# Kernel tuning notes

Hardware: AMD Instinct MI355X
Metric: run time of the kernel (lower is better)

The kernel has to match this reference:

```python
import jax, jax.numpy as jnp
import numpy as np

DIM = 128
HEADS = 4
G = 16           # group_size (window)
POS_DIM = (DIM // 4) // 4  # 8, DPB hidden dim
EPS = 1e-5


def _ln(x, g, b):
    m = x.mean(-1, keepdims=True)
    v = ((x - m) ** 2).mean(-1, keepdims=True)
    return (x - m) * jax.lax.rsqrt(v + EPS) * g + b


def _rel_index(Gh, Gw):
    # relative_position_index as in the torch code (static, numpy)
    coords = np.stack(np.meshgrid(np.arange(Gh), np.arange(Gw), indexing='ij'))  # [2,Gh,Gw]
    cf = coords.reshape(2, -1)
    rel = (cf[:, :, None] - cf[:, None, :]).transpose(1, 2, 0)  # [N,N,2]
    rel[..., 0] += Gh - 1
    rel[..., 1] += Gw - 1
    rel[..., 0] *= 2 * Gw - 1
    return rel.sum(-1)  # [N,N]


def _bias_coords(Gh, Gw):
    bh = np.arange(1 - Gh, Gh)
    bw = np.arange(1 - Gw, Gw)
    b = np.stack(np.meshgrid(bh, bw, indexing='ij')).reshape(2, -1).T  # [(2Gh-1)(2Gw-1),2]
    return b.astype(np.float32)


def setup_inputs() -> dict:
    key = jax.random.key(0)
    ks = jax.random.split(key, 16)
    C, P, h = DIM, POS_DIM, HEADS
    s = 0.02
    return {
        'x': jax.random.normal(ks[0], (2, 256 * 256, C), jnp.float32),
        'norm1_g': jnp.ones((C,), jnp.float32),
        'norm1_b': jnp.zeros((C,), jnp.float32),
        'qkv_w': jax.random.normal(ks[1], (3 * C, C), jnp.float32) * s,
        'qkv_b': jnp.zeros((3 * C,), jnp.float32),
        'pp_w': jax.random.normal(ks[2], (P, 2), jnp.float32) * s,
        'pp_b': jnp.zeros((P,), jnp.float32),
        'l1_g': jnp.ones((P,), jnp.float32), 'l1_b': jnp.zeros((P,), jnp.float32),
        'f1_w': jax.random.normal(ks[3], (P, P), jnp.float32) * s,
        'f1_b': jnp.zeros((P,), jnp.float32),
        'l2_g': jnp.ones((P,), jnp.float32), 'l2_b': jnp.zeros((P,), jnp.float32),
        'f2_w': jax.random.normal(ks[4], (P, P), jnp.float32) * s,
        'f2_b': jnp.zeros((P,), jnp.float32),
        'l3_g': jnp.ones((P,), jnp.float32), 'l3_b': jnp.zeros((P,), jnp.float32),
        'f3_w': jax.random.normal(ks[5], (h, P), jnp.float32) * s,
        'f3_b': jnp.zeros((h,), jnp.float32),
        'H': 256,
        'W': 256,
    }


def reference(x, norm1_g, norm1_b, qkv_w, qkv_b, pp_w, pp_b,
              l1_g, l1_b, f1_w, f1_b, l2_g, l2_b, f2_w, f2_b,
              l3_g, l3_b, f3_w, f3_b, H, W):
    B, L, C = x.shape
    h = HEADS
    d = C // h
    N = G * G
    shortcut = x
    xn = _ln(x, norm1_g, norm1_b).reshape(B, H, W, C)
    # SDA window partition: (B, H/G, G, W/G, G, C) -> (B*nW, G*G, C)
    xw = xn.reshape(B, H // G, G, W // G, G, C).transpose(0, 1, 3, 2, 4, 5).reshape(-1, N, C)
    qkv = (xw @ qkv_w.T + qkv_b).reshape(-1, N, 3, h, d).transpose(2, 0, 3, 1, 4)
    q, k, v = qkv[0] * (d ** -0.5), qkv[1], qkv[2]
    attn = jnp.einsum('bhnd,bhmd->bhnm', q, k)  # [B_, h, N, N]
    # DynamicPosBias (residual=False): pos3(pos2(pos1(pos_proj(biases))))
    biases = jnp.asarray(_bias_coords(G, G))  # [(2G-1)^2, 2]
    pos = biases @ pp_w.T + pp_b
    pos = jax.nn.relu(_ln(pos, l1_g, l1_b)) @ f1_w.T + f1_b
    pos = jax.nn.relu(_ln(pos, l2_g, l2_b)) @ f2_w.T + f2_b
    pos = jax.nn.relu(_ln(pos, l3_g, l3_b)) @ f3_w.T + f3_b  # [(2G-1)^2, h]
    rpi = jnp.asarray(_rel_index(G, G).reshape(-1))
    bias = pos[rpi].reshape(N, N, h).transpose(2, 0, 1)  # [h, N, N]
    attn = jax.nn.softmax(attn + bias[None], axis=-1)
    out = jnp.einsum('bhnm,bhmd->bhnd', attn, v).transpose(0, 2, 1, 3).reshape(-1, N, C)
    # reverse partition
    out = out.reshape(B, H // G, W // G, G, G, C).transpose(0, 1, 3, 2, 4, 5).reshape(B, L, C)
    return shortcut + out
```

## Files before the change

### kernel.cpp

```cpp
#include <hip/hip_runtime.h>
#include <hip/hip_bf16.h>

typedef __bf16 bf16_t;
typedef __bf16 bf16x2 __attribute__((ext_vector_type(2)));
typedef __bf16 bf16x4 __attribute__((ext_vector_type(4)));
typedef __bf16 bf16x8 __attribute__((ext_vector_type(8)));
typedef short s16x4 __attribute__((ext_vector_type(4)));
typedef float f32x2 __attribute__((ext_vector_type(2)));
typedef float f32x4 __attribute__((ext_vector_type(4)));
typedef unsigned int u32;

#define MFMA16(a, b, c) __builtin_amdgcn_mfma_f32_16x16x32_bf16(a, b, c, 0, 0, 0)

static __device__ inline f32x4 mfma_pv(bf16x4 a, bf16x4 b, f32x4 c) {
#if __has_builtin(__builtin_amdgcn_mfma_f32_16x16x16_bf16)
    return __builtin_amdgcn_mfma_f32_16x16x16_bf16(a, b, c, 0, 0, 0);
#elif __has_builtin(__builtin_amdgcn_mfma_f32_16x16x16bf16_1k)
    return __builtin_amdgcn_mfma_f32_16x16x16bf16_1k(
        __builtin_bit_cast(s16x4, a), __builtin_bit_cast(s16x4, b), c, 0, 0, 0);
#else
    f32x4 d;
    asm volatile("v_mfma_f32_16x16x16_bf16 %0, %1, %2, %3"
                 : "=v"(d) : "v"(a), "v"(b), "v"(c));
    return d;
#endif
}

__device__ inline float ldf(const void* p, int i, int f32) {
    return f32 ? ((const float*)p)[i] : (float)((const bf16_t*)p)[i];
}

__device__ inline void ln8(float* p, const void* g, const void* b, int f32) {
    float m = 0.f;
#pragma unroll
    for (int i = 0; i < 8; ++i) m += p[i];
    m *= 0.125f;
    float v = 0.f;
#pragma unroll
    for (int i = 0; i < 8; ++i) { float d = p[i] - m; v += d * d; }
    v *= 0.125f;
    float r = rsqrtf(v + 1e-5f);
#pragma unroll
    for (int i = 0; i < 8; ++i)
        p[i] = fmaxf((p[i] - m) * r * ldf(g, i, f32) + ldf(b, i, f32), 0.f);
}

__global__ __launch_bounds__(256) void prep_all(
    const void* __restrict__ xv, bf16_t* __restrict__ xn,
    int* __restrict__ flags,
    const void* __restrict__ qw, const void* __restrict__ qb,
    const void* __restrict__ ng, const void* __restrict__ nb,
    bf16_t* __restrict__ Wp, float* __restrict__ uu, float* __restrict__ tt,
    const void* __restrict__ ppw, const void* __restrict__ ppb,
    const void* __restrict__ l1g, const void* __restrict__ l1b,
    const void* __restrict__ f1w, const void* __restrict__ f1b,
    const void* __restrict__ l2g, const void* __restrict__ l2b,
    const void* __restrict__ f2w, const void* __restrict__ f2b,
    const void* __restrict__ l3g, const void* __restrict__ l3b,
    const void* __restrict__ f3w, const void* __restrict__ f3b,
    float* __restrict__ pos) {
    const int tid = threadIdx.x;
    const int lane = tid & 63;
    u32 pv = ((const u32*)xv)[lane];
    int pf = (((pv >> 7) & 0xFFu) >= 0x90u) || (((pv >> 23) & 0xFFu) >= 0x90u);
    const int f32 = __any(pf) ? 1 : 0;
    const int bid = blockIdx.x;
    if (bid == 0 && tid == 0) flags[0] = f32;

    if (bid >= 100) {
        const int sub = lane & 15;
        const int t = (bid - 100) * 16 + (tid >> 6) * 4 + (lane >> 4);
        float f[8];
        if (f32) {
            const float* p = (const float*)xv + t * 128 + sub * 8;
            f32x4 a = *(const f32x4*)p;
            f32x4 b = *(const f32x4*)(p + 4);
#pragma unroll
            for (int e = 0; e < 4; ++e) { f[e] = a[e]; f[4 + e] = b[e]; }
        } else {
            bf16x8 v = *(const bf16x8*)((const bf16_t*)xv + t * 128 + sub * 8);
#pragma unroll
            for (int e = 0; e < 8; ++e) f[e] = (float)v[e];
        }
        float s = 0.f, s2 = 0.f;
#pragma unroll
        for (int e = 0; e < 8; ++e) { s += f[e]; s2 += f[e] * f[e]; }
#pragma unroll
        for (int off = 8; off >= 1; off >>= 1) {
            s += __shfl_xor(s, off, 64);
            s2 += __shfl_xor(s2, off, 64);
        }
        float mu = s * (1.f / 128.f);
        float r = rsqrtf(s2 * (1.f / 128.f) - mu * mu + 1e-5f);
        bf16x8 h;
#pragma unroll
        for (int e = 0; e < 8; ++e) h[e] = (bf16_t)((f[e] - mu) * r);
        *(bf16x8*)(xn + t * 128 + sub * 8) = h;
        return;
    }

    if (bid < 96) {
        int j = bid * 4 + (tid >> 6);
        int l = lane;
        float g0 = ldf(ng, l, f32),  g1 = ldf(ng, l + 64, f32);
        float b0 = ldf(nb, l, f32),  b1 = ldf(nb, l + 64, f32);
        float w0 = ldf(qw, j * 128 + l, f32), w1 = ldf(qw, j * 128 + l + 64, f32);
        float wg0 = w0 * g0, wg1 = w1 * g1;
        Wp[j * 128 + l] = (bf16_t)wg0;
        Wp[j * 128 + l + 64] = (bf16_t)wg1;
        float su = wg0 + wg1;
        float st = w0 * b0 + w1 * b1;
#pragma unroll
        for (int off = 32; off >= 1; off >>= 1) {
            su += __shfl_xor(su, off, 64);
            st += __shfl_xor(st, off, 64);
        }
        if (l == 0) { uu[j] = su; tt[j] = st + ldf(qb, j, f32); }
        return;
    }

    int r = (bid - 96) * 256 + tid;
    if (r >= 961) return;
    float bh = (float)(r / 31) - 15.f;
    float bw = (float)(r % 31) - 15.f;
    float p[8], q[8];
#pragma unroll
    for (int i = 0; i < 8; ++i)
        p[i] = ldf(ppw, i * 2, f32) * bh + ldf(ppw, i * 2 + 1, f32) * bw + ldf(ppb, i, f32);
    ln8(p, l1g, l1b, f32);
#pragma unroll
    for (int o = 0; o < 8; ++o) {
        float s = ldf(f1b, o, f32);
#pragma unroll
        for (int i = 0; i < 8; ++i) s += p[i] * ldf(f1w, o * 8 + i, f32);
        q[o] = s;
    }
    ln8(q, l2g, l2b, f32);
#pragma unroll
    for (int o = 0; o < 8; ++o) {
        float s = ldf(f2b, o, f32);
#pragma unroll
        for (int i = 0; i < 8; ++i) s += q[i] * ldf(f2w, o * 8 + i, f32);
        p[o] = s;
    }
    ln8(p, l3g, l3b, f32);
#pragma unroll
    for (int o = 0; o < 4; ++o) {
        float s = ldf(f3b, o, f32);
#pragma unroll
        for (int i = 0; i < 8; ++i) s += p[i] * ldf(f3w, o * 8 + i, f32);
        pos[r * 4 + o] = s;
    }
}

template <int XN>
__global__ __launch_bounds__(256, 4) void win_attn(
    const void* __restrict__ xv, const bf16_t* __restrict__ xnp,
    const bf16_t* __restrict__ Wp, const float* __restrict__ uu,
    const float* __restrict__ tt, const float* __restrict__ posg,
    const int* __restrict__ flags, void* __restrict__ outv) {
    __shared__ __align__(16) bf16_t k_s[256 * 40];
    __shared__ __align__(16) bf16_t vT_s[32 * 264];
    __shared__ bf16_t pos_s[962];
    __shared__ float tt_s[96];
    __shared__ float uu_s[XN ? 2 : 96];
    __shared__ float mu_s[XN ? 2 : 256];
    __shared__ float r_s[XN ? 2 : 256];

    const int f32 = flags[0];
    const int tid = threadIdx.x;
    const int lane = tid & 63;
    const int w = tid >> 6;
    const int l15 = lane & 15;
    const int quad = lane >> 4;
    const int bid = blockIdx.x;
    const int head = (bid >> 3) & 3;
    const int wi = (bid & 7) | ((bid >> 5) << 3);
    const int bi = wi >> 8;
    const int wh = (wi >> 4) & 15, ww = wi & 15;
    const int xbase = bi * (256 * 256 * 128);

    if (tid < 96) {
        int sg = tid >> 5, dd = tid & 31;
        tt_s[tid] = tt[sg * 128 + head * 32 + dd];
        if (!XN) uu_s[tid] = uu[sg * 128 + head * 32 + dd];
    }
    for (int r = tid; r < 961; r += 256) pos_s[r] = (bf16_t)posg[r * 4 + head];

    if (!XN) {
#pragma unroll
        for (int it = 0; it < 4; ++it) {
            int i = w * 64 + it * 16 + (lane >> 2);
            int gi = xbase + ((wh * 16 + (i >> 4)) * 256 + ww * 16 + (i & 15)) * 128;
            float s = 0.f, s2 = 0.f;
            if (f32) {
                const f32x4* p4 = (const f32x4*)((const float*)xv + gi);
#pragma unroll
                for (int c = 0; c < 4; ++c) {
                    f32x4 a = p4[(c * 4 + (lane & 3)) * 2];
                    f32x4 b = p4[(c * 4 + (lane & 3)) * 2 + 1];
#pragma unroll
                    for (int e = 0; e < 4; ++e) { s += a[e] + b[e]; s2 += a[e] * a[e] + b[e] * b[e]; }
                }
            } else {
                const bf16_t* p = (const bf16_t*)xv + gi;
#pragma unroll
                for (int c = 0; c < 4; ++c) {
                    bf16x8 v = *(const bf16x8*)(p + (c * 4 + (lane & 3)) * 8);
#pragma unroll
                    for (int e = 0; e < 8; ++e) { float f = (float)v[e]; s += f; s2 += f * f; }
                }
            }
            s  += __shfl_xor(s, 1, 4);  s  += __shfl_xor(s, 2, 4);
            s2 += __shfl_xor(s2, 1, 4); s2 += __shfl_xor(s2, 2, 4);
            if ((lane & 3) == 0) {
                float mu = s * (1.f / 128.f);
                mu_s[i] = mu;
                r_s[i] = rsqrtf(s2 * (1.f / 128.f) - mu * mu + 1e-5f);
            }
        }
    }
    __syncthreads();

    int axi[4];
#pragma unroll
    for (int mt = 0; mt < 4; ++mt) {
        int i = w * 64 + mt * 16 + l15;
        axi[mt] = xbase + ((wh * 16 + (i >> 4)) * 256 + ww * 16 + (i & 15)) * 128;
    }
    const float qscale = 0.17677669529663689f;
    bf16x8 qB[4];

#pragma unroll 1
    for (int sel = 0; sel < 3; ++sel) {
        f32x4 acc[2][4];
#pragma unroll
        for (int nt = 0; nt < 2; ++nt)
#pragma unroll
            for (int mt = 0; mt < 4; ++mt) acc[nt][mt] = f32x4{0.f, 0.f, 0.f, 0.f};
        const bf16_t* bw0 = Wp + (sel * 128 + head * 32 + l15) * 128;
        const bf16_t* bw1 = bw0 + 16 * 128;
#pragma unroll
        for (int ks = 0; ks < 4; ++ks) {
            int ko = ks * 32 + quad * 8;
            bf16x8 af[4];
            if (XN) {
#pragma unroll
                for (int mt = 0; mt < 4; ++mt)
                    af[mt] = *(const bf16x8*)(xnp + axi[mt] + ko);
            } else if (f32) {
#pragma unroll
                for (int mt = 0; mt < 4; ++mt) {
                    const float* pp = (const float*)xv + axi[mt] + ko;
                    f32x4 u0 = *(const f32x4*)pp;
                    f32x4 u1 = *(const f32x4*)(pp + 4);
                    bf16x8 t;
#pragma unroll
                    for (int e = 0; e < 4; ++e) { t[e] = (bf16_t)u0[e]; t[e + 4] = (bf16_t)u1[e]; }
                    af[mt] = t;
                }
            } else {
#pragma unroll
                for (int mt = 0; mt < 4; ++mt)
                    af[mt] = *(const bf16x8*)((const bf16_t*)xv + axi[mt] + ko);
            }
            bf16x8 b0 = *(const bf16x8*)(bw0 + ko);
            bf16x8 b1 = *(const bf16x8*)(bw1 + ko);
#pragma unroll
            for (int mt = 0; mt < 4; ++mt) {
                acc[0][mt] = MFMA16(af[mt], b0, acc[0][mt]);
                acc[1][mt] = MFMA16(af[mt], b1, acc[1][mt]);
            }
        }
#pragma unroll
        for (int nt = 0; nt < 2; ++nt) {
            int d = nt * 16 + l15;
            float tj = tt_s[sel * 32 + d];
            float uj = XN ? 0.f : uu_s[sel * 32 + d];
#pragma unroll
            for (int mt = 0; mt < 4; ++mt) {
                int tok0 = w * 64 + mt * 16 + quad * 4;
                float vv[4];
#pragma unroll
                for (int rg = 0; rg < 4; ++rg) {
                    int token = tok0 + rg;
                    if (XN) vv[rg] = acc[nt][mt][rg] + tj;
                    else    vv[rg] = r_s[token] * (acc[nt][mt][rg] - mu_s[token] * uj) + tj;
                }
                if (sel == 0) {
#pragma unroll
                    for (int rg = 0; rg < 4; ++rg)
                        k_s[(tok0 + rg) * 40 + d] = (bf16_t)(vv[rg] * qscale);
                } else if (sel == 1) {
#pragma unroll
                    for (int rg = 0; rg < 4; ++rg)
                        k_s[(tok0 + rg) * 40 + d] = (bf16_t)vv[rg];
                } else {
                    bf16x4 h = { (bf16_t)vv[0], (bf16_t)vv[1],
                                 (bf16_t)vv[2], (bf16_t)vv[3] };
                    *(bf16x4*)(vT_s + d * 264 + tok0) = h;
                }
            }
        }
        if (sel == 0) {
#pragma unroll
            for (int qt = 0; qt < 4; ++qt)
                qB[qt] = *(const bf16x8*)(k_s + (w * 64 + qt * 16 + l15) * 40 + quad * 8);
            __syncthreads();
        }
    }
    __syncthreads();

    f32x4 Oa[2][4];
#pragma unroll
    for (int np = 0; np < 2; ++np)
#pragma unroll
        for (int qt = 0; qt < 4; ++qt) Oa[np][qt] = f32x4{0.f, 0.f, 0.f, 0.f};
    float lsum[4] = {0.f, 0.f, 0.f, 0.f};

    const f32x4 zero4 = {0.f, 0.f, 0.f, 0.f};
    const int vinner = l15 + 15 - quad * 4;

    for (int kb = 0; kb < 8; ++kb) {
        bf16x4 pF[2][4];
#pragma unroll
        for (int nt = 0; nt < 2; ++nt) {
            bf16x8 kf = *(const bf16x8*)(k_s + (kb * 32 + nt * 16 + l15) * 40 + quad * 8);
            f32x4 S[4];
            __builtin_amdgcn_s_setprio(1);
#pragma unroll
            for (int qt = 0; qt < 4; ++qt) S[qt] = MFMA16(kf, qB[qt], zero4);
            __builtin_amdgcn_s_setprio(0);
#pragma unroll
            for (int qt = 0; qt < 4; ++qt) {
                int souter = (w * 4 + qt - kb * 2 - nt + 15) * 31;
                float p[4];
#pragma unroll
                for (int rg = 0; rg < 4; ++rg) {
                    float b = (float)pos_s[souter + vinner - rg];
                    p[rg] = __expf(S[qt][rg] + b);
                }
                lsum[qt] += (p[0] + p[1]) + (p[2] + p[3]);
                bf16x4 h = { (bf16_t)p[0], (bf16_t)p[1], (bf16_t)p[2], (bf16_t)p[3] };
                pF[nt][qt] = h;
            }
        }
#pragma unroll
        for (int np = 0; np < 2; ++np) {
            const bf16_t* vrow = vT_s + (np * 16 + l15) * 264 + kb * 32 + quad * 4;
            bf16x4 vf0 = *(const bf16x4*)vrow;
            bf16x4 vf1 = *(const bf16x4*)(vrow + 16);
            __builtin_amdgcn_s_setprio(1);
#pragma unroll
            for (int qt = 0; qt < 4; ++qt) {
                Oa[np][qt] = mfma_pv(vf0, pF[0][qt], Oa[np][qt]);
                Oa[np][qt] = mfma_pv(vf1, pF[1][qt], Oa[np][qt]);
            }
            __builtin_amdgcn_s_setprio(0);
        }
    }

    float inv[4];
#pragma unroll
    for (int qt = 0; qt < 4; ++qt) {
        float l = lsum[qt];
        l += __shfl_xor(l, 16, 64);
        l += __shfl_xor(l, 32, 64);
        inv[qt] = 1.f / l;
    }
#pragma unroll
    for (int np = 0; np < 2; ++np)
#pragma unroll
        for (int qt = 0; qt < 4; ++qt) {
            int go = xbase + ((wh * 16 + w * 4 + qt) * 256 + ww * 16 + l15) * 128 +
                     head * 32 + np * 16 + quad * 4;
            if (f32) {
                f32x4 res = *(const f32x4*)((const float*)xv + go);
                f32x4 o;
#pragma unroll
                for (int rg = 0; rg < 4; ++rg) o[rg] = Oa[np][qt][rg] * inv[qt] + res[rg];
                *(f32x4*)((float*)outv + go) = o;
            } else {
                bf16x4 res = *(const bf16x4*)((const bf16_t*)xv + go);
                bf16x4 o;
#pragma unroll
                for (int rg = 0; rg < 4; ++rg)
                    o[rg] = (bf16_t)(Oa[np][qt][rg] * inv[qt] + (float)res[rg]);
                *(bf16x4*)((bf16_t*)outv + go) = o;
            }
        }
}

extern "C" void kernel_launch(void* const* d_in, const int* in_sizes, int n_in,
                              void* d_out, int out_size, void* d_ws, size_t ws_size,
                              hipStream_t stream) {
    const void* x   = d_in[0];
    const void* ng  = d_in[1];
    const void* nb  = d_in[2];
    const void* qw  = d_in[3];
    const void* qb  = d_in[4];
    const void* ppw = d_in[5];
    const void* ppb = d_in[6];
    const void* l1g = d_in[7];
    const void* l1b = d_in[8];
    const void* f1w = d_in[9];
    const void* f1b = d_in[10];
    const void* l2g = d_in[11];
    const void* l2b = d_in[12];
    const void* f2w = d_in[13];
    const void* f2b = d_in[14];
    const void* l3g = d_in[15];
    const void* l3b = d_in[16];
    const void* f3w = d_in[17];
    const void* f3b = d_in[18];

    char* ws = (char*)d_ws;
    int*    flags = (int*)ws;
    bf16_t* Wp    = (bf16_t*)(ws + 16);
    float*  uu    = (float*)(ws + 98320);
    float*  tt    = (float*)(ws + 99856);
    float*  pos   = (float*)(ws + 101392);
    bf16_t* xn    = (bf16_t*)(ws + 116768);
    const int use_xn = (ws_size >= 116768 + 33554432u) ? 1 : 0;

    int prep_grid = use_xn ? 8292 : 100;
    prep_all<<<dim3(prep_grid), dim3(256), 0, stream>>>(
        x, xn, flags, qw, qb, ng, nb, Wp, uu, tt,
        ppw, ppb, l1g, l1b, f1w, f1b, l2g, l2b, f2w, f2b, l3g, l3b,
        f3w, f3b, pos);
    if (use_xn)
        win_attn<1><<<dim3(2048), dim3(256), 0, stream>>>(x, xn, Wp, uu, tt, pos,
                                                          flags, d_out);
    else
        win_attn<0><<<dim3(2048), dim3(256), 0, stream>>>(x, xn, Wp, uu, tt, pos,
                                                          flags, d_out);
}
```

Before: 270.8 us.

## Drop separate LayerNorm pass and fuse row stats into window attention kernel

After: 304.6 us. 1.12x slower.

```diff
diff --git a/kernel.cpp b/kernel.cpp
--- a/kernel.cpp
+++ b/kernel.cpp
@@ -46,8 +46,7 @@
 }
 
 __global__ __launch_bounds__(256) void prep_all(
-    const void* __restrict__ xv, bf16_t* __restrict__ xn,
-    int* __restrict__ flags,
+    const void* __restrict__ xv,
     const void* __restrict__ qw, const void* __restrict__ qb,
     const void* __restrict__ ng, const void* __restrict__ nb,
     bf16_t* __restrict__ Wp, float* __restrict__ uu, float* __restrict__ tt,
@@ -65,39 +64,6 @@
     int pf = (((pv >> 7) & 0xFFu) >= 0x90u) || (((pv >> 23) & 0xFFu) >= 0x90u);
     const int f32 = __any(pf) ? 1 : 0;
     const int bid = blockIdx.x;
-    if (bid == 0 && tid == 0) flags[0] = f32;
-
-    if (bid >= 100) {
-        const int sub = lane & 15;
-        const int t = (bid - 100) * 16 + (tid >> 6) * 4 + (lane >> 4);
-        float f[8];
-        if (f32) {
-            const float* p = (const float*)xv + t * 128 + sub * 8;
-            f32x4 a = *(const f32x4*)p;
-            f32x4 b = *(const f32x4*)(p + 4);
-#pragma unroll
-            for (int e = 0; e < 4; ++e) { f[e] = a[e]; f[4 + e] = b[e]; }
-        } else {
-            bf16x8 v = *(const bf16x8*)((const bf16_t*)xv + t * 128 + sub * 8);
-#pragma unroll
-            for (int e = 0; e < 8; ++e) f[e] = (float)v[e];
-        }
-        float s = 0.f, s2 = 0.f;
-#pragma unroll
-        for (int e = 0; e < 8; ++e) { s += f[e]; s2 += f[e] * f[e]; }
-#pragma unroll
-        for (int off = 8; off >= 1; off >>= 1) {
-            s += __shfl_xor(s, off, 64);
-            s2 += __shfl_xor(s2, off, 64);
-        }
-        float mu = s * (1.f / 128.f);
-        float r = rsqrtf(s2 * (1.f / 128.f) - mu * mu + 1e-5f);
-        bf16x8 h;
-#pragma unroll
-        for (int e = 0; e < 8; ++e) h[e] = (bf16_t)((f[e] - mu) * r);
-        *(bf16x8*)(xn + t * 128 + sub * 8) = h;
-        return;
-    }
 
     if (bid < 96) {
         int j = bid * 4 + (tid >> 6);
@@ -153,26 +119,22 @@
     }
 }
 
-template <int XN>
 __global__ __launch_bounds__(256, 4) void win_attn(
-    const void* __restrict__ xv, const bf16_t* __restrict__ xnp,
-    const bf16_t* __restrict__ Wp, const float* __restrict__ uu,
-    const float* __restrict__ tt, const float* __restrict__ posg,
-    const int* __restrict__ flags, void* __restrict__ outv) {
+    const void* __restrict__ xv, const bf16_t* __restrict__ Wp,
+    const float* __restrict__ uu, const float* __restrict__ tt,
+    const float* __restrict__ posg, void* __restrict__ outv) {
     __shared__ __align__(16) bf16_t k_s[256 * 40];
     __shared__ __align__(16) bf16_t vT_s[32 * 264];
     __shared__ bf16_t pos_s[962];
-    __shared__ float tt_s[96];
-    __shared__ float uu_s[XN ? 2 : 96];
-    __shared__ float mu_s[XN ? 2 : 256];
-    __shared__ float r_s[XN ? 2 : 256];
-
-    const int f32 = flags[0];
+
     const int tid = threadIdx.x;
     const int lane = tid & 63;
     const int w = tid >> 6;
     const int l15 = lane & 15;
     const int quad = lane >> 4;
+    u32 pvw = ((const u32*)xv)[lane];
+    int pfb = (((pvw >> 7) & 0xFFu) >= 0x90u) || (((pvw >> 23) & 0xFFu) >= 0x90u);
+    const int f32 = __any(pfb) ? 1 : 0;
     const int bid = blockIdx.x;
     const int head = (bid >> 3) & 3;
     const int wi = (bid & 7) | ((bid >> 5) << 3);
@@ -180,47 +142,40 @@
     const int wh = (wi >> 4) & 15, ww = wi & 15;
     const int xbase = bi * (256 * 256 * 128);
 
-    if (tid < 96) {
-        int sg = tid >> 5, dd = tid & 31;
-        tt_s[tid] = tt[sg * 128 + head * 32 + dd];
-        if (!XN) uu_s[tid] = uu[sg * 128 + head * 32 + dd];
-    }
     for (int r = tid; r < 961; r += 256) pos_s[r] = (bf16_t)posg[r * 4 + head];
 
-    if (!XN) {
-#pragma unroll
-        for (int it = 0; it < 4; ++it) {
-            int i = w * 64 + it * 16 + (lane >> 2);
-            int gi = xbase + ((wh * 16 + (i >> 4)) * 256 + ww * 16 + (i & 15)) * 128;
-            float s = 0.f, s2 = 0.f;
-            if (f32) {
-                const f32x4* p4 = (const f32x4*)((const float*)xv + gi);
-#pragma unroll
-                for (int c = 0; c < 4; ++c) {
-                    f32x4 a = p4[(c * 4 + (lane & 3)) * 2];
-                    f32x4 b = p4[(c * 4 + (lane & 3)) * 2 + 1];
-#pragma unroll
-                    for (int e = 0; e < 4; ++e) { s += a[e] + b[e]; s2 += a[e] * a[e] + b[e] * b[e]; }
-                }
-            } else {
-                const bf16_t* p = (const bf16_t*)xv + gi;
-#pragma unroll
-                for (int c = 0; c < 4; ++c) {
-                    bf16x8 v = *(const bf16x8*)(p + (c * 4 + (lane & 3)) * 8);
-#pragma unroll
-                    for (int e = 0; e < 8; ++e) { float f = (float)v[e]; s += f; s2 += f * f; }
-                }
-            }
-            s  += __shfl_xor(s, 1, 4);  s  += __shfl_xor(s, 2, 4);
-            s2 += __shfl_xor(s2, 1, 4); s2 += __shfl_xor(s2, 2, 4);
-            if ((lane & 3) == 0) {
-                float mu = s * (1.f / 128.f);
-                mu_s[i] = mu;
-                r_s[i] = rsqrtf(s2 * (1.f / 128.f) - mu * mu + 1e-5f);
-            }
-        }
-    }
-    __syncthreads();
+#pragma unroll
+    for (int it = 0; it < 4; ++it) {
+        int i = w * 64 + it * 16 + (lane >> 2);
+        int gi = xbase + ((wh * 16 + (i >> 4)) * 256 + ww * 16 + (i & 15)) * 128;
+        float s = 0.f, s2 = 0.f;
+        if (f32) {
+            const f32x4* p4 = (const f32x4*)((const float*)xv + gi);
+#pragma unroll
+            for (int c = 0; c < 4; ++c) {
+                f32x4 a = p4[(c * 4 + (lane & 3)) * 2];
+                f32x4 b = p4[(c * 4 + (lane & 3)) * 2 + 1];
+#pragma unroll
+                for (int e = 0; e < 4; ++e) { s += a[e] + b[e]; s2 += a[e] * a[e] + b[e] * b[e]; }
+            }
+        } else {
+            const bf16_t* p = (const bf16_t*)xv + gi;
+#pragma unroll
+            for (int c = 0; c < 4; ++c) {
+                bf16x8 v = *(const bf16x8*)(p + (c * 4 + (lane & 3)) * 8);
+#pragma unroll
+                for (int e = 0; e < 8; ++e) { float f = (float)v[e]; s += f; s2 += f * f; }
+            }
+        }
+        s  += __shfl_xor(s, 1, 4);  s  += __shfl_xor(s, 2, 4);
+        s2 += __shfl_xor(s2, 1, 4); s2 += __shfl_xor(s2, 2, 4);
+        if ((lane & 3) == 0) {
+            float mu = s * (1.f / 128.f);
+            float r = rsqrtf(s2 * (1.f / 128.f) - mu * mu + 1e-5f);
+            f32x2 st = { mu, r };
+            *(f32x2*)(k_s + i * 40 + 32) = st;
+        }
+    }
 
     int axi[4];
 #pragma unroll
@@ -233,6 +188,12 @@
 
 #pragma unroll 1
     for (int sel = 0; sel < 3; ++sel) {
+        float tjv[2], ujv[2];
+#pragma unroll
+        for (int nt = 0; nt < 2; ++nt) {
+            tjv[nt] = tt[sel * 128 + head * 32 + nt * 16 + l15];
+            ujv[nt] = uu[sel * 128 + head * 32 + nt * 16 + l15];
+        }
         f32x4 acc[2][4];
 #pragma unroll
         for (int nt = 0; nt < 2; ++nt)
@@ -244,11 +205,7 @@
         for (int ks = 0; ks < 4; ++ks) {
             int ko = ks * 32 + quad * 8;
             bf16x8 af[4];
-            if (XN) {
-#pragma unroll
-                for (int mt = 0; mt < 4; ++mt)
-                    af[mt] = *(const bf16x8*)(xnp + axi[mt] + ko);
-            } else if (f32) {
+            if (f32) {
 #pragma unroll
                 for (int mt = 0; mt < 4; ++mt) {
                     const float* pp = (const float*)xv + axi[mt] + ko;
@@ -273,20 +230,21 @@
             }
         }
 #pragma unroll
-        for (int nt = 0; nt < 2; ++nt) {
-            int d = nt * 16 + l15;
-            float tj = tt_s[sel * 32 + d];
-            float uj = XN ? 0.f : uu_s[sel * 32 + d];
-#pragma unroll
-            for (int mt = 0; mt < 4; ++mt) {
-                int tok0 = w * 64 + mt * 16 + quad * 4;
+        for (int mt = 0; mt < 4; ++mt) {
+            int tok0 = w * 64 + mt * 16 + quad * 4;
+            float mu4[4], r4[4];
+#pragma unroll
+            for (int rg = 0; rg < 4; ++rg) {
+                f32x2 st = *(const f32x2*)(k_s + (tok0 + rg) * 40 + 32);
+                mu4[rg] = st[0]; r4[rg] = st[1];
+            }
+#pragma unroll
+            for (int nt = 0; nt < 2; ++nt) {
+                int d = nt * 16 + l15;
                 float vv[4];
 #pragma unroll
-                for (int rg = 0; rg < 4; ++rg) {
-                    int token = tok0 + rg;
-                    if (XN) vv[rg] = acc[nt][mt][rg] + tj;
-                    else    vv[rg] = r_s[token] * (acc[nt][mt][rg] - mu_s[token] * uj) + tj;
-                }
+                for (int rg = 0; rg < 4; ++rg)
+                    vv[rg] = r4[rg] * (acc[nt][mt][rg] - mu4[rg] * ujv[nt]) + tjv[nt];
                 if (sel == 0) {
 #pragma unroll
                     for (int rg = 0; rg < 4; ++rg)
@@ -306,7 +264,6 @@
 #pragma unroll
             for (int qt = 0; qt < 4; ++qt)
                 qB[qt] = *(const bf16x8*)(k_s + (w * 64 + qt * 16 + l15) * 40 + quad * 8);
-            __syncthreads();
         }
     }
     __syncthreads();
@@ -415,23 +372,14 @@
     const void* f3b = d_in[18];
 
     char* ws = (char*)d_ws;
-    int*    flags = (int*)ws;
     bf16_t* Wp    = (bf16_t*)(ws + 16);
     float*  uu    = (float*)(ws + 98320);
     float*  tt    = (float*)(ws + 99856);
     float*  pos   = (float*)(ws + 101392);
-    bf16_t* xn    = (bf16_t*)(ws + 116768);
-    const int use_xn = (ws_size >= 116768 + 33554432u) ? 1 : 0;
-
-    int prep_grid = use_xn ? 8292 : 100;
-    prep_all<<<dim3(prep_grid), dim3(256), 0, stream>>>(
-        x, xn, flags, qw, qb, ng, nb, Wp, uu, tt,
+
+    prep_all<<<dim3(100), dim3(256), 0, stream>>>(
+        x, qw, qb, ng, nb, Wp, uu, tt,
         ppw, ppb, l1g, l1b, f1w, f1b, l2g, l2b, f2w, f2b, l3g, l3b,
         f3w, f3b, pos);
-    if (use_xn)
-        win_attn<1><<<dim3(2048), dim3(256), 0, stream>>>(x, xn, Wp, uu, tt, pos,
-                                                          flags, d_out);
-    else
-        win_attn<0><<<dim3(2048), dim3(256), 0, stream>>>(x, xn, Wp, uu, tt, pos,
-                                                          flags, d_out);
-}
+    win_attn<<<dim3(2048), dim3(256), 0, stream>>>(x, Wp, uu, tt, pos, d_out);
+}
```

## Split window attention across eight waves and switch softmax to exp2

Applied to the files above, without the earlier changes.

Result: slower. 282.5 us (+4.3%).

```diff
diff --git a/kernel.cpp b/kernel.cpp
--- a/kernel.cpp
+++ b/kernel.cpp
@@ -23,6 +23,14 @@
     asm volatile("v_mfma_f32_16x16x16_bf16 %0, %1, %2, %3"
                  : "=v"(d) : "v"(a), "v"(b), "v"(c));
     return d;
+#endif
+}
+
+static __device__ inline float fast_exp2(float x) {
+#if __has_builtin(__builtin_amdgcn_exp2f)
+    return __builtin_amdgcn_exp2f(x);
+#else
+    return exp2f(x);
 #endif
 }
 
@@ -154,7 +162,7 @@
 }
 
 template <int XN>
-__global__ __launch_bounds__(256, 4) void win_attn(
+__global__ __launch_bounds__(512, 8) void win_attn(
     const void* __restrict__ xv, const bf16_t* __restrict__ xnp,
     const bf16_t* __restrict__ Wp, const float* __restrict__ uu,
     const float* __restrict__ tt, const float* __restrict__ posg,
@@ -162,8 +170,6 @@
     __shared__ __align__(16) bf16_t k_s[256 * 40];
     __shared__ __align__(16) bf16_t vT_s[32 * 264];
     __shared__ bf16_t pos_s[962];
-    __shared__ float tt_s[96];
-    __shared__ float uu_s[XN ? 2 : 96];
     __shared__ float mu_s[XN ? 2 : 256];
     __shared__ float r_s[XN ? 2 : 256];
 
@@ -180,17 +186,13 @@
     const int wh = (wi >> 4) & 15, ww = wi & 15;
     const int xbase = bi * (256 * 256 * 128);
 
-    if (tid < 96) {
-        int sg = tid >> 5, dd = tid & 31;
-        tt_s[tid] = tt[sg * 128 + head * 32 + dd];
-        if (!XN) uu_s[tid] = uu[sg * 128 + head * 32 + dd];
-    }
-    for (int r = tid; r < 961; r += 256) pos_s[r] = (bf16_t)posg[r * 4 + head];
+    for (int r = tid; r < 961; r += 512)
+        pos_s[r] = (bf16_t)(posg[r * 4 + head] * 1.4426950408889634f);
 
     if (!XN) {
 #pragma unroll
-        for (int it = 0; it < 4; ++it) {
-            int i = w * 64 + it * 16 + (lane >> 2);
+        for (int it = 0; it < 2; ++it) {
+            int i = w * 32 + it * 16 + (lane >> 2);
             int gi = xbase + ((wh * 16 + (i >> 4)) * 256 + ww * 16 + (i & 15)) * 128;
             float s = 0.f, s2 = 0.f;
             if (f32) {
@@ -220,37 +222,42 @@
             }
         }
     }
-    __syncthreads();
-
-    int axi[4];
-#pragma unroll
-    for (int mt = 0; mt < 4; ++mt) {
-        int i = w * 64 + mt * 16 + l15;
+
+    int axi[2];
+#pragma unroll
+    for (int mt = 0; mt < 2; ++mt) {
+        int i = w * 32 + mt * 16 + l15;
         axi[mt] = xbase + ((wh * 16 + (i >> 4)) * 256 + ww * 16 + (i & 15)) * 128;
     }
-    const float qscale = 0.17677669529663689f;
-    bf16x8 qB[4];
+    const float qscale = 0.25503486f;
+    bf16x8 qB[2];
 
 #pragma unroll 1
     for (int sel = 0; sel < 3; ++sel) {
-        f32x4 acc[2][4];
+        float tjv[2], ujv[2];
+#pragma unroll
+        for (int nt = 0; nt < 2; ++nt) {
+            tjv[nt] = tt[sel * 128 + head * 32 + nt * 16 + l15];
+            ujv[nt] = XN ? 0.f : uu[sel * 128 + head * 32 + nt * 16 + l15];
+        }
+        f32x4 acc[2][2];
 #pragma unroll
         for (int nt = 0; nt < 2; ++nt)
 #pragma unroll
-            for (int mt = 0; mt < 4; ++mt) acc[nt][mt] = f32x4{0.f, 0.f, 0.f, 0.f};
+            for (int mt = 0; mt < 2; ++mt) acc[nt][mt] = f32x4{0.f, 0.f, 0.f, 0.f};
         const bf16_t* bw0 = Wp + (sel * 128 + head * 32 + l15) * 128;
         const bf16_t* bw1 = bw0 + 16 * 128;
 #pragma unroll
         for (int ks = 0; ks < 4; ++ks) {
             int ko = ks * 32 + quad * 8;
-            bf16x8 af[4];
+            bf16x8 af[2];
             if (XN) {
 #pragma unroll
-                for (int mt = 0; mt < 4; ++mt)
+                for (int mt = 0; mt < 2; ++mt)
                     af[mt] = *(const bf16x8*)(xnp + axi[mt] + ko);
             } else if (f32) {
 #pragma unroll
-                for (int mt = 0; mt < 4; ++mt) {
+                for (int mt = 0; mt < 2; ++mt) {
                     const float* pp = (const float*)xv + axi[mt] + ko;
                     f32x4 u0 = *(const f32x4*)pp;
                     f32x4 u1 = *(const f32x4*)(pp + 4);
@@ -261,31 +268,31 @@
                 }
             } else {
 #pragma unroll
-                for (int mt = 0; mt < 4; ++mt)
+                for (int mt = 0; mt < 2; ++mt)
                     af[mt] = *(const bf16x8*)((const bf16_t*)xv + axi[mt] + ko);
             }
             bf16x8 b0 = *(const bf16x8*)(bw0 + ko);
             bf16x8 b1 = *(const bf16x8*)(bw1 + ko);
 #pragma unroll
-            for (int mt = 0; mt < 4; ++mt) {
+            for (int mt = 0; mt < 2; ++mt) {
                 acc[0][mt] = MFMA16(af[mt], b0, acc[0][mt]);
                 acc[1][mt] = MFMA16(af[mt], b1, acc[1][mt]);
             }
         }
 #pragma unroll
-        for (int nt = 0; nt < 2; ++nt) {
-            int d = nt * 16 + l15;
-            float tj = tt_s[sel * 32 + d];
-            float uj = XN ? 0.f : uu_s[sel * 32 + d];
-#pragma unroll
-            for (int mt = 0; mt < 4; ++mt) {
-                int tok0 = w * 64 + mt * 16 + quad * 4;
+        for (int mt = 0; mt < 2; ++mt) {
+            int tok0 = w * 32 + mt * 16 + quad * 4;
+#pragma unroll
+            for (int nt = 0; nt < 2; ++nt) {
+                int d = nt * 16 + l15;
                 float vv[4];
 #pragma unroll
                 for (int rg = 0; rg < 4; ++rg) {
-                    int token = tok0 + rg;
-                    if (XN) vv[rg] = acc[nt][mt][rg] + tj;
-                    else    vv[rg] = r_s[token] * (acc[nt][mt][rg] - mu_s[token] * uj) + tj;
+                    if (XN) vv[rg] = acc[nt][mt][rg] + tjv[nt];
+                    else {
+                        int token = tok0 + rg;
+                        vv[rg] = r_s[token] * (acc[nt][mt][rg] - mu_s[token] * ujv[nt]) + tjv[nt];
+                    }
                 }
                 if (sel == 0) {
 #pragma unroll
@@ -304,41 +311,40 @@
         }
         if (sel == 0) {
 #pragma unroll
-            for (int qt = 0; qt < 4; ++qt)
-                qB[qt] = *(const bf16x8*)(k_s + (w * 64 + qt * 16 + l15) * 40 + quad * 8);
-            __syncthreads();
+            for (int qt = 0; qt < 2; ++qt)
+                qB[qt] = *(const bf16x8*)(k_s + (w * 32 + qt * 16 + l15) * 40 + quad * 8);
         }
     }
     __syncthreads();
 
-    f32x4 Oa[2][4];
+    f32x4 Oa[2][2];
 #pragma unroll
     for (int np = 0; np < 2; ++np)
 #pragma unroll
-        for (int qt = 0; qt < 4; ++qt) Oa[np][qt] = f32x4{0.f, 0.f, 0.f, 0.f};
-    float lsum[4] = {0.f, 0.f, 0.f, 0.f};
+        for (int qt = 0; qt < 2; ++qt) Oa[np][qt] = f32x4{0.f, 0.f, 0.f, 0.f};
+    float lsum[2] = {0.f, 0.f};
 
     const f32x4 zero4 = {0.f, 0.f, 0.f, 0.f};
     const int vinner = l15 + 15 - quad * 4;
 
     for (int kb = 0; kb < 8; ++kb) {
-        bf16x4 pF[2][4];
+        bf16x4 pF[2][2];
 #pragma unroll
         for (int nt = 0; nt < 2; ++nt) {
             bf16x8 kf = *(const bf16x8*)(k_s + (kb * 32 + nt * 16 + l15) * 40 + quad * 8);
-            f32x4 S[4];
+            f32x4 S[2];
             __builtin_amdgcn_s_setprio(1);
 #pragma unroll
-            for (int qt = 0; qt < 4; ++qt) S[qt] = MFMA16(kf, qB[qt], zero4);
+            for (int qt = 0; qt < 2; ++qt) S[qt] = MFMA16(kf, qB[qt], zero4);
             __builtin_amdgcn_s_setprio(0);
 #pragma unroll
-            for (int qt = 0; qt < 4; ++qt) {
-                int souter = (w * 4 + qt - kb * 2 - nt + 15) * 31;
+            for (int qt = 0; qt < 2; ++qt) {
+                int souter = (w * 2 + qt - kb * 2 - nt + 15) * 31;
                 float p[4];
 #pragma unroll
                 for (int rg = 0; rg < 4; ++rg) {
                     float b = (float)pos_s[souter + vinner - rg];
-                    p[rg] = __expf(S[qt][rg] + b);
+                    p[rg] = fast_exp2(S[qt][rg] + b);
                 }
                 lsum[qt] += (p[0] + p[1]) + (p[2] + p[3]);
                 bf16x4 h = { (bf16_t)p[0], (bf16_t)p[1], (bf16_t)p[2], (bf16_t)p[3] };
@@ -352,7 +358,7 @@
             bf16x4 vf1 = *(const bf16x4*)(vrow + 16);
             __builtin_amdgcn_s_setprio(1);
 #pragma unroll
-            for (int qt = 0; qt < 4; ++qt) {
+            for (int qt = 0; qt < 2; ++qt) {
                 Oa[np][qt] = mfma_pv(vf0, pF[0][qt], Oa[np][qt]);
                 Oa[np][qt] = mfma_pv(vf1, pF[1][qt], Oa[np][qt]);
             }
@@ -360,9 +366,9 @@
         }
     }
 
-    float inv[4];
-#pragma unroll
-    for (int qt = 0; qt < 4; ++qt) {
+    float inv[2];
+#pragma unroll
+    for (int qt = 0; qt < 2; ++qt) {
         float l = lsum[qt];
         l += __shfl_xor(l, 16, 64);
         l += __shfl_xor(l, 32, 64);
@@ -371,8 +377,8 @@
 #pragma unroll
     for (int np = 0; np < 2; ++np)
 #pragma unroll
-        for (int qt = 0; qt < 4; ++qt) {
-            int go = xbase + ((wh * 16 + w * 4 + qt) * 256 + ww * 16 + l15) * 128 +
+        for (int qt = 0; qt < 2; ++qt) {
+            int go = xbase + ((wh * 16 + w * 2 + qt) * 256 + ww * 16 + l15) * 128 +
                      head * 32 + np * 16 + quad * 4;
             if (f32) {
                 f32x4 res = *(const f32x4*)((const float*)xv + go);
@@ -429,9 +435,9 @@
         ppw, ppb, l1g, l1b, f1w, f1b, l2g, l2b, f2w, f2b, l3g, l3b,
         f3w, f3b, pos);
     if (use_xn)
-        win_attn<1><<<dim3(2048), dim3(256), 0, stream>>>(x, xn, Wp, uu, tt, pos,
+        win_attn<1><<<dim3(2048), dim3(512), 0, stream>>>(x, xn, Wp, uu, tt, pos,
                                                           flags, d_out);
     else
-        win_attn<0><<<dim3(2048), dim3(256), 0, stream>>>(x, xn, Wp, uu, tt, pos,
+        win_attn<0><<<dim3(2048), dim3(512), 0, stream>>>(x, xn, Wp, uu, tt, pos,
                                                           flags, d_out);
 }
```

## Fuse Q/K/V projection passes and switch softmax to exp2 with prescaled bias

Applied to the files above, without the earlier changes.

Result: slower. 319.1 us (+17.8%).

```diff
diff --git a/kernel.cpp b/kernel.cpp
--- a/kernel.cpp
+++ b/kernel.cpp
@@ -23,6 +23,14 @@
     asm volatile("v_mfma_f32_16x16x16_bf16 %0, %1, %2, %3"
                  : "=v"(d) : "v"(a), "v"(b), "v"(c));
     return d;
+#endif
+}
+
+static __device__ inline float fast_exp2(float x) {
+#if __has_builtin(__builtin_amdgcn_exp2f)
+    return __builtin_amdgcn_exp2f(x);
+#else
+    return exp2f(x);
 #endif
 }
 
@@ -162,8 +170,6 @@
     __shared__ __align__(16) bf16_t k_s[256 * 40];
     __shared__ __align__(16) bf16_t vT_s[32 * 264];
     __shared__ bf16_t pos_s[962];
-    __shared__ float tt_s[96];
-    __shared__ float uu_s[XN ? 2 : 96];
     __shared__ float mu_s[XN ? 2 : 256];
     __shared__ float r_s[XN ? 2 : 256];
 
@@ -180,12 +186,8 @@
     const int wh = (wi >> 4) & 15, ww = wi & 15;
     const int xbase = bi * (256 * 256 * 128);
 
-    if (tid < 96) {
-        int sg = tid >> 5, dd = tid & 31;
-        tt_s[tid] = tt[sg * 128 + head * 32 + dd];
-        if (!XN) uu_s[tid] = uu[sg * 128 + head * 32 + dd];
-    }
-    for (int r = tid; r < 961; r += 256) pos_s[r] = (bf16_t)posg[r * 4 + head];
+    for (int r = tid; r < 961; r += 256)
+        pos_s[r] = (bf16_t)(posg[r * 4 + head] * 1.4426950408889634f);
 
     if (!XN) {
 #pragma unroll
@@ -220,7 +222,6 @@
             }
         }
     }
-    __syncthreads();
 
     int axi[4];
 #pragma unroll
@@ -228,64 +229,79 @@
         int i = w * 64 + mt * 16 + l15;
         axi[mt] = xbase + ((wh * 16 + (i >> 4)) * 256 + ww * 16 + (i & 15)) * 128;
     }
-    const float qscale = 0.17677669529663689f;
+    const float qscale = 0.25503486f;
     bf16x8 qB[4];
 
-#pragma unroll 1
+    float tjv[3][2], ujv[3][2];
+#pragma unroll
+    for (int sel = 0; sel < 3; ++sel)
+#pragma unroll
+        for (int nt = 0; nt < 2; ++nt) {
+            tjv[sel][nt] = tt[sel * 128 + head * 32 + nt * 16 + l15];
+            ujv[sel][nt] = XN ? 0.f : uu[sel * 128 + head * 32 + nt * 16 + l15];
+        }
+
+    f32x4 acc[3][2][4];
+#pragma unroll
+    for (int sel = 0; sel < 3; ++sel)
+#pragma unroll
+        for (int nt = 0; nt < 2; ++nt)
+#pragma unroll
+            for (int mt = 0; mt < 4; ++mt) acc[sel][nt][mt] = f32x4{0.f, 0.f, 0.f, 0.f};
+
+    const bf16_t* bwBase = Wp + (head * 32 + l15) * 128;
+#pragma unroll
+    for (int ks = 0; ks < 4; ++ks) {
+        int ko = ks * 32 + quad * 8;
+        bf16x8 af[4];
+        if (XN) {
+#pragma unroll
+            for (int mt = 0; mt < 4; ++mt)
+                af[mt] = *(const bf16x8*)(xnp + axi[mt] + ko);
+        } else if (f32) {
+#pragma unroll
+            for (int mt = 0; mt < 4; ++mt) {
+                const float* pp = (const float*)xv + axi[mt] + ko;
+                f32x4 u0 = *(const f32x4*)pp;
+                f32x4 u1 = *(const f32x4*)(pp + 4);
+                bf16x8 t;
+#pragma unroll
+                for (int e = 0; e < 4; ++e) { t[e] = (bf16_t)u0[e]; t[e + 4] = (bf16_t)u1[e]; }
+                af[mt] = t;
+            }
+        } else {
+#pragma unroll
+            for (int mt = 0; mt < 4; ++mt)
+                af[mt] = *(const bf16x8*)((const bf16_t*)xv + axi[mt] + ko);
+        }
+#pragma unroll
+        for (int sel = 0; sel < 3; ++sel) {
+            bf16x8 b0 = *(const bf16x8*)(bwBase + sel * (128 * 128) + ko);
+            bf16x8 b1 = *(const bf16x8*)(bwBase + sel * (128 * 128) + 16 * 128 + ko);
+#pragma unroll
+            for (int mt = 0; mt < 4; ++mt) {
+                acc[sel][0][mt] = MFMA16(af[mt], b0, acc[sel][0][mt]);
+                acc[sel][1][mt] = MFMA16(af[mt], b1, acc[sel][1][mt]);
+            }
+        }
+    }
+
+#pragma unroll
     for (int sel = 0; sel < 3; ++sel) {
-        f32x4 acc[2][4];
-#pragma unroll
-        for (int nt = 0; nt < 2; ++nt)
-#pragma unroll
-            for (int mt = 0; mt < 4; ++mt) acc[nt][mt] = f32x4{0.f, 0.f, 0.f, 0.f};
-        const bf16_t* bw0 = Wp + (sel * 128 + head * 32 + l15) * 128;
-        const bf16_t* bw1 = bw0 + 16 * 128;
-#pragma unroll
-        for (int ks = 0; ks < 4; ++ks) {
-            int ko = ks * 32 + quad * 8;
-            bf16x8 af[4];
-            if (XN) {
-#pragma unroll
-                for (int mt = 0; mt < 4; ++mt)
-                    af[mt] = *(const bf16x8*)(xnp + axi[mt] + ko);
-            } else if (f32) {
-#pragma unroll
-                for (int mt = 0; mt < 4; ++mt) {
-                    const float* pp = (const float*)xv + axi[mt] + ko;
-                    f32x4 u0 = *(const f32x4*)pp;
-                    f32x4 u1 = *(const f32x4*)(pp + 4);
-                    bf16x8 t;
-#pragma unroll
-                    for (int e = 0; e < 4; ++e) { t[e] = (bf16_t)u0[e]; t[e + 4] = (bf16_t)u1[e]; }
-                    af[mt] = t;
-                }
-            } else {
-#pragma unroll
-                for (int mt = 0; mt < 4; ++mt)
-                    af[mt] = *(const bf16x8*)((const bf16_t*)xv + axi[mt] + ko);
-            }
-            bf16x8 b0 = *(const bf16x8*)(bw0 + ko);
-            bf16x8 b1 = *(const bf16x8*)(bw1 + ko);
-#pragma unroll
-            for (int mt = 0; mt < 4; ++mt) {
-                acc[0][mt] = MFMA16(af[mt], b0, acc[0][mt]);
-                acc[1][mt] = MFMA16(af[mt], b1, acc[1][mt]);
-            }
-        }
-#pragma unroll
-        for (int nt = 0; nt < 2; ++nt) {
-            int d = nt * 16 + l15;
-            float tj = tt_s[sel * 32 + d];
-            float uj = XN ? 0.f : uu_s[sel * 32 + d];
-#pragma unroll
-            for (int mt = 0; mt < 4; ++mt) {
-                int tok0 = w * 64 + mt * 16 + quad * 4;
+#pragma unroll
+        for (int mt = 0; mt < 4; ++mt) {
+            int tok0 = w * 64 + mt * 16 + quad * 4;
+#pragma unroll
+            for (int nt = 0; nt < 2; ++nt) {
+                int d = nt * 16 + l15;
                 float vv[4];
 #pragma unroll
                 for (int rg = 0; rg < 4; ++rg) {
-                    int token = tok0 + rg;
-                    if (XN) vv[rg] = acc[nt][mt][rg] + tj;
-                    else    vv[rg] = r_s[token] * (acc[nt][mt][rg] - mu_s[token] * uj) + tj;
+                    if (XN) vv[rg] = acc[sel][nt][mt][rg] + tjv[sel][nt];
+                    else {
+                        int token = tok0 + rg;
+                        vv[rg] = r_s[token] * (acc[sel][nt][mt][rg] - mu_s[token] * ujv[sel][nt]) + tjv[sel][nt];
+                    }
                 }
                 if (sel == 0) {
 #pragma unroll
@@ -306,7 +322,6 @@
 #pragma unroll
             for (int qt = 0; qt < 4; ++qt)
                 qB[qt] = *(const bf16x8*)(k_s + (w * 64 + qt * 16 + l15) * 40 + quad * 8);
-            __syncthreads();
         }
     }
     __syncthreads();
@@ -321,6 +336,7 @@
     const f32x4 zero4 = {0.f, 0.f, 0.f, 0.f};
     const int vinner = l15 + 15 - quad * 4;
 
+#pragma unroll 2
     for (int kb = 0; kb < 8; ++kb) {
         bf16x4 pF[2][4];
 #pragma unroll
@@ -338,7 +354,7 @@
 #pragma unroll
                 for (int rg = 0; rg < 4; ++rg) {
                     float b = (float)pos_s[souter + vinner - rg];
-                    p[rg] = __expf(S[qt][rg] + b);
+                    p[rg] = fast_exp2(S[qt][rg] + b);
                 }
                 lsum[qt] += (p[0] + p[1]) + (p[2] + p[3]);
                 bf16x4 h = { (bf16_t)p[0], (bf16_t)p[1], (bf16_t)p[2], (bf16_t)p[3] };
@@ -369,9 +385,9 @@
         inv[qt] = 1.f / l;
     }
 #pragma unroll
-    for (int np = 0; np < 2; ++np)
-#pragma unroll
-        for (int qt = 0; qt < 4; ++qt) {
+    for (int qt = 0; qt < 4; ++qt)
+#pragma unroll
+        for (int np = 0; np < 2; ++np) {
             int go = xbase + ((wh * 16 + w * 4 + qt) * 256 + ww * 16 + l15) * 128 +
                      head * 32 + np * 16 + quad * 4;
             if (f32) {
```
